# Kernel tuning notes

Measured on AMD Instinct MI355X. Metric: run time of the kernel, lower is better.

## Reference

```python
import jax, jax.numpy as jnp
import numpy as np

B, L, D = 4, 4096, 1024
H = 16
HD = D // H                      # 64
WIN = 256
MLP_RATIO = 4.0
FFN = int(2 * int(D * MLP_RATIO) / 3)   # 2730
EPS = 1e-6


def setup_inputs() -> dict:
    key = jax.random.key(0)
    ks = jax.random.split(key, 16)
    s = 0.02
    return {
        "x": jax.random.normal(ks[0], (B, L, D), jnp.float32),
        "c": jax.random.normal(ks[1], (B, D), jnp.float32),
        "norm1_scale": jnp.ones((D,), jnp.float32),
        "norm2_scale": jnp.ones((D,), jnp.float32),
        "adaLN_w": jax.random.normal(ks[2], (D, 6 * D), jnp.float32) * s,
        "adaLN_b": jnp.zeros((6 * D,), jnp.float32),
        "qkv_w": jax.random.normal(ks[3], (D, 3 * D), jnp.float32) * s,
        "qkv_b": jnp.zeros((3 * D,), jnp.float32),
        "out_proj_w": jax.random.normal(ks[4], (D, D), jnp.float32) * s,
        "out_proj_b": jnp.zeros((D,), jnp.float32),
        "w12_w": jax.random.normal(ks[5], (D, 2 * FFN), jnp.float32) * s,
        "w12_b": jnp.zeros((2 * FFN,), jnp.float32),
        "w3_w": jax.random.normal(ks[6], (FFN, D), jnp.float32) * s,
        "w3_b": jnp.zeros((D,), jnp.float32),
    }


def _rmsnorm(x, scale):
    xf = x.astype(jnp.float32)
    var = jnp.mean(jnp.square(xf), axis=-1, keepdims=True)
    xn = (xf * jax.lax.rsqrt(var + EPS)).astype(x.dtype)
    return xn * scale


def _modulation(x, shift, scale):
    return x * (1.0 + scale[:, None, :]) + shift[:, None, :]


def _rope(x):
    # Faithful to original: seq axis is x.shape[-2], which here is the HEAD axis.
    seq_len, hd = x.shape[-2], x.shape[-1]
    theta = 10000.0
    freqs = 1.0 / theta ** (jnp.arange(0, hd, 2, dtype=jnp.float32) / hd)
    t = jnp.arange(seq_len, dtype=jnp.float32)
    freqs_cis = jnp.einsum("i,j->ij", t, freqs)        # (seq, hd/2)
    sin = jnp.repeat(jnp.sin(freqs_cis), 2, axis=-1)   # (seq, hd)
    cos = jnp.repeat(jnp.cos(freqs_cis), 2, axis=-1)
    x1, x2 = jnp.split(x, 2, axis=-1)
    rot = jnp.concatenate([-x2, x1], axis=-1)
    return x * cos + rot * sin


def reference(x, c, norm1_scale, norm2_scale, adaLN_w, adaLN_b,
              qkv_w, qkv_b, out_proj_w, out_proj_b,
              w12_w, w12_b, w3_w, w3_b):
    # adaLN modulation params from conditioning
    ada = jax.nn.silu(c) @ adaLN_w + adaLN_b                      # (B, 6D)
    sh_msa, sc_msa, g_msa, sh_mlp, sc_mlp, g_mlp = jnp.split(ada, 6, axis=-1)

    # --- attention branch ---
    res = x
    xm = _modulation(_rmsnorm(x, norm1_scale), sh_msa, sc_msa)    # (B,L,D)
    nw = L // WIN
    xw = xm.reshape(B * nw, WIN, D)
    qkv = xw @ qkv_w + qkv_b
    q, k, v = jnp.split(qkv, 3, axis=-1)
    q = q.reshape(B * nw, WIN, H, HD)
    k = k.reshape(B * nw, WIN, H, HD)
    v = v.reshape(B * nw, WIN, H, HD)
    q, k = _rope(q), _rope(k)
    scores = jnp.einsum("bqhd,bkhd->bhqk", q, k) / jnp.sqrt(jnp.float32(HD))
    attn = jax.nn.softmax(scores, axis=-1)
    out = jnp.einsum("bhqk,bkhd->bqhd", attn, v).reshape(B, L, D)
    out = out @ out_proj_w + out_proj_b
    x = res + g_msa[:, None, :] * out

    # --- MLP branch ---
    res = x
    xm = _modulation(_rmsnorm(x, norm2_scale), sh_mlp, sc_mlp)
    w12 = xm @ w12_w + w12_b                                      # (B,L,2*FFN)
    w1, w2 = jnp.split(w12, 2, axis=-1)
    mlp = (jax.nn.silu(w1) * w2) @ w3_w + w3_b
    return res + g_mlp[:, None, :] * mlp
```

## Files before the change

kernel.cpp:

```cpp
#include <hip/hip_runtime.h>
#include <hip/hip_bf16.h>
#include <cstdint>
#include <cstddef>

#define DEV __device__ __forceinline__

typedef float f32x4 __attribute__((ext_vector_type(4)));
typedef short s16x8 __attribute__((ext_vector_type(8)));
typedef short s16x4 __attribute__((ext_vector_type(4)));
typedef __bf16 bf16x8 __attribute__((ext_vector_type(8)));

DEV unsigned short f2bf(float f) {
  union { float f; unsigned u; } v; v.f = f;
  return (unsigned short)((v.u + 0x7FFFu + ((v.u >> 16) & 1u)) >> 16);
}
DEV float bf2f(unsigned short s) {
  union { unsigned u; float f; } v; v.u = ((unsigned)s) << 16;
  return v.f;
}

DEV void mfma16(f32x4& d, const s16x8& a, const s16x8& b) {
  d = __builtin_amdgcn_mfma_f32_16x16x32_bf16(
      __builtin_bit_cast(bf16x8, a), __builtin_bit_cast(bf16x8, b), d, 0, 0, 0);
}

typedef const unsigned int gu32 __attribute__((address_space(1)));
typedef unsigned int lu32 __attribute__((address_space(3)));
DEV void gl_lds16(const void* g, void* l) {
  __builtin_amdgcn_global_load_lds((gu32*)g, (lu32*)l, 16, 0, 0);
}

__global__ void transpose_w(const float* __restrict__ src, int srcLd, int K,
                            int colOff, int nCols,
                            unsigned short* __restrict__ dst, int dstLd, int rowOff,
                            int ilv)
{
  __shared__ float tile[32][33];
  int tx = threadIdx.x & 31, ty = threadIdx.x >> 5;
  int k0 = blockIdx.y * 32, n0 = blockIdx.x * 32;
#pragma unroll
  for (int r = 0; r < 4; ++r) {
    int kk = k0 + ty + r * 8;
    int nn = n0 + tx;
    if (kk < K && nn < nCols) tile[ty + r * 8][tx] = src[(size_t)kk * srcLd + colOff + nn];
  }
  __syncthreads();
#pragma unroll
  for (int r = 0; r < 4; ++r) {
    int nn = n0 + ty + r * 8;
    int kk = k0 + tx;
    if (nn < nCols && kk < K) {
      int row = ilv ? (((nn >> 4) << 5) + (nn & 15) + rowOff) : (rowOff + nn);
      dst[(size_t)row * dstLd + kk] = f2bf(tile[tx][ty + r * 8]);
    }
  }
}

__global__ void biaspad_kernel(const float* __restrict__ b, float* __restrict__ out)
{
  int n = blockIdx.x * 256 + threadIdx.x;
  if (n >= 5632) return;
  int bb = n >> 4, i = n & 15;
  int src = ((bb >> 1) << 4) + i;
  float v = 0.f;
  if (src < 2730) v = (bb & 1) ? b[2730 + src] : b[src];
  out[n] = v;
}

__global__ void ada_kernel(const float* __restrict__ c, const float* __restrict__ w,
                           const float* __restrict__ b, float* __restrict__ ada)
{
  __shared__ float cs[1024];
  int bb = blockIdx.y;
  int j = blockIdx.x * 256 + threadIdx.x;
  for (int i = threadIdx.x; i < 1024; i += 256) {
    float v = c[bb * 1024 + i];
    cs[i] = v / (1.f + __expf(-v));
  }
  __syncthreads();
  float acc = b[j];
  for (int k = 0; k < 1024; ++k) acc = fmaf(cs[k], w[(size_t)k * 6144 + j], acc);
  ada[bb * 6144 + j] = acc;
}

__global__ void rmsmod_kernel(const float* __restrict__ x, const float* __restrict__ nsc,
                              const float* __restrict__ ada, int shOff, int scOff,
                              unsigned short* __restrict__ out)
{
  int row = blockIdx.x;
  int t = threadIdx.x;
  const f32x4* xr = (const f32x4*)(x + (size_t)row * 1024);
  f32x4 v = xr[t];
  float ss = v[0]*v[0] + v[1]*v[1] + v[2]*v[2] + v[3]*v[3];
#pragma unroll
  for (int off = 32; off >= 1; off >>= 1) ss += __shfl_xor(ss, off, 64);
  __shared__ float red[4];
  int lane = t & 63, wv = t >> 6;
  if (lane == 0) red[wv] = ss;
  __syncthreads();
  float tot = red[0] + red[1] + red[2] + red[3];
  float rms = rsqrtf(tot * (1.f / 1024.f) + 1e-6f);
  int bb = row >> 12;
  const float* ab = ada + bb * 6144;
  s16x4 o;
#pragma unroll
  for (int i = 0; i < 4; ++i) {
    int col = t * 4 + i;
    float xn = v[i] * rms * nsc[col];
    float val = xn * (1.f + ab[scOff + col]) + ab[shOff + col];
    o[i] = (short)f2bf(val);
  }
  *(s16x4*)(out + (size_t)row * 1024 + t * 4) = o;
}

template<int EPI>
__global__ __launch_bounds__(512, 2) void gemm256(
    const unsigned short* __restrict__ A, int lda,
    const unsigned short* __restrict__ BT, int ldb,
    int N, int K,
    const float* __restrict__ bias,
    void* __restrict__ Cout, int Nout,
    const float* __restrict__ res,
    const float* __restrict__ ada, int gateOff)
{
  __shared__ __align__(16) char lds[131072];

  const int tid = threadIdx.x;
  const int lane = tid & 63;
  const int wv = tid >> 6;
  const int wr = wv >> 2;
  const int wn = wv & 3;
  const int g = lane >> 4, r16 = lane & 15;

  const int nwg = gridDim.x * gridDim.y;
  const int bid = blockIdx.x + gridDim.x * blockIdx.y;
  const int qq = nwg >> 3;
  const int swz = (bid & 7) * qq + (bid >> 3);
  const int m0 = (swz / gridDim.x) * 256;
  const int n0 = (swz % gridDim.x) * 256;

  const int nkt = K >> 6;

  auto stageB = [&](int t) {
    if (t >= nkt) return;
    const int bs = t & 1;
#pragma unroll
    for (int it = 0; it < 4; ++it) {
      const int cidx = it * 512 + tid;
      const int rl = cidx >> 3, cc = cidx & 7;
      const unsigned short* src =
          BT + (size_t)(n0 + rl) * ldb + t * 64 + ((cc ^ (rl & 7)) << 3);
      gl_lds16(src, lds + 65536 + bs * 32768 + cidx * 16);
    }
  };
  auto stageA = [&](int t) {
    if (t >= nkt) return;
    const int bs = t & 1;
#pragma unroll
    for (int it = 0; it < 4; ++it) {
      const int cidx = it * 512 + tid;
      const int rl = cidx >> 3, cc = cidx & 7;
      const unsigned short* src =
          A + (size_t)(m0 + rl) * lda + t * 64 + ((cc ^ (rl & 7)) << 3);
      gl_lds16(src, lds + bs * 32768 + cidx * 16);
    }
  };

  f32x4 acc[8][4];
#pragma unroll
  for (int m = 0; m < 8; ++m)
#pragma unroll
    for (int n = 0; n < 4; ++n) { acc[m][n][0]=0.f; acc[m][n][1]=0.f; acc[m][n][2]=0.f; acc[m][n][3]=0.f; }

  int swzk[2];
#pragma unroll
  for (int ks = 0; ks < 2; ++ks) swzk[ks] = (((ks << 2) + g) ^ (r16 & 7)) << 4;
  int arow0[4], arow1[4], brow0[2], brow1[2];
#pragma unroll
  for (int m = 0; m < 4; ++m) {
    arow0[m] = (wr * 128 + m * 16 + r16) * 128;
    arow1[m] = (wr * 128 + 64 + m * 16 + r16) * 128;
  }
#pragma unroll
  for (int n = 0; n < 2; ++n) {
    brow0[n] = 65536 + (wn * 64 + n * 16 + r16) * 128;
    brow1[n] = 65536 + (wn * 64 + 32 + n * 16 + r16) * 128;
  }

  stageB(0); stageA(0); stageB(1); stageA(1);
  asm volatile("s_waitcnt vmcnt(8)" ::: "memory");
  __builtin_amdgcn_s_barrier();

  for (int kt = 0; kt < nkt; ++kt) {
    const int boff = (kt & 1) * 32768;
    s16x8 a0[4][2], a1[4][2], b0[2][2], b1[2][2];
#pragma unroll
    for (int m = 0; m < 4; ++m)
#pragma unroll
      for (int ks = 0; ks < 2; ++ks)
        a0[m][ks] = *(const s16x8*)(lds + boff + arow0[m] + swzk[ks]);
#pragma unroll
    for (int n = 0; n < 2; ++n)
#pragma unroll
      for (int ks = 0; ks < 2; ++ks)
        b0[n][ks] = *(const s16x8*)(lds + boff + brow0[n] + swzk[ks]);
#pragma unroll
    for (int n = 0; n < 2; ++n)
#pragma unroll
      for (int ks = 0; ks < 2; ++ks)
        b1[n][ks] = *(const s16x8*)(lds + boff + brow1[n] + swzk[ks]);
#pragma unroll
    for (int m = 0; m < 4; ++m)
#pragma unroll
      for (int ks = 0; ks < 2; ++ks)
        a1[m][ks] = *(const s16x8*)(lds + boff + arow1[m] + swzk[ks]);
    __builtin_amdgcn_s_setprio(1);
#pragma unroll
    for (int m = 0; m < 4; ++m)
#pragma unroll
      for (int n = 0; n < 2; ++n)
#pragma unroll
        for (int ks = 0; ks < 2; ++ks)
          mfma16(acc[m][n], a0[m][ks], b0[n][ks]);
    __builtin_amdgcn_s_setprio(0);
    __builtin_amdgcn_s_setprio(1);
#pragma unroll
    for (int m = 0; m < 4; ++m)
#pragma unroll
      for (int n = 0; n < 2; ++n)
#pragma unroll
        for (int ks = 0; ks < 2; ++ks)
          mfma16(acc[m][2 + n], a0[m][ks], b1[n][ks]);
    __builtin_amdgcn_s_setprio(0);
    __builtin_amdgcn_s_barrier();
    stageB(kt + 2);
    __builtin_amdgcn_s_setprio(1);
#pragma unroll
    for (int m = 0; m < 4; ++m)
#pragma unroll
      for (int n = 0; n < 2; ++n)
#pragma unroll
        for (int ks = 0; ks < 2; ++ks)
          mfma16(acc[4 + m][2 + n], a1[m][ks], b1[n][ks]);
    __builtin_amdgcn_s_setprio(0);
    if (kt + 2 < nkt) asm volatile("s_waitcnt vmcnt(4)" ::: "memory");
    else              asm volatile("s_waitcnt vmcnt(0)" ::: "memory");
    __builtin_amdgcn_s_barrier();
    stageA(kt + 2);
    __builtin_amdgcn_s_setprio(1);
#pragma unroll
    for (int m = 0; m < 4; ++m)
#pragma unroll
      for (int n = 0; n < 2; ++n)
#pragma unroll
        for (int ks = 0; ks < 2; ++ks)
          mfma16(acc[4 + m][n], a1[m][ks], b0[n][ks]);
    __builtin_amdgcn_s_setprio(0);
  }

  if (EPI == 0) {
    unsigned short* Co = (unsigned short*)Cout;
#pragma unroll
    for (int fm = 0; fm < 8; ++fm)
#pragma unroll
      for (int fn = 0; fn < 4; ++fn)
#pragma unroll
        for (int r = 0; r < 4; ++r) {
          int rg = m0 + wr * 128 + fm * 16 + g * 4 + r;
          int cg = n0 + wn * 64 + fn * 16 + r16;
          Co[(size_t)rg * Nout + cg] = f2bf(acc[fm][fn][r] + bias[cg]);
        }
  } else if (EPI == 1) {
    unsigned short* Co = (unsigned short*)Cout;
#pragma unroll
    for (int fm = 0; fm < 8; ++fm)
#pragma unroll
      for (int p = 0; p < 2; ++p)
#pragma unroll
        for (int r = 0; r < 4; ++r) {
          int rg = m0 + wr * 128 + fm * 16 + g * 4 + r;
          int cg = n0 + wn * 64 + (2 * p) * 16 + r16;
          float v1 = acc[fm][2 * p][r] + bias[cg];
          float v2 = acc[fm][2 * p + 1][r] + bias[cg + 16];
          float h = v1 / (1.f + __expf(-v1)) * v2;
          int hcol = (n0 >> 1) + wn * 32 + p * 16 + r16;
          Co[(size_t)rg * Nout + hcol] = f2bf(h);
        }
  } else {
    float* Co = (float*)Cout;
#pragma unroll
    for (int fm = 0; fm < 8; ++fm)
#pragma unroll
      for (int fn = 0; fn < 4; ++fn)
#pragma unroll
        for (int r = 0; r < 4; ++r) {
          int rg = m0 + wr * 128 + fm * 16 + g * 4 + r;
          int cg = n0 + wn * 64 + fn * 16 + r16;
          float v = acc[fm][fn][r] + bias[cg];
          int bb = rg >> 12;
          float gate = ada[bb * 6144 + gateOff + cg];
          size_t idx = (size_t)rg * Nout + cg;
          Co[idx] = res[idx] + gate * v;
        }
  }
}

template<int MODE>
__global__ void gemm128(const unsigned short* __restrict__ A, int lda,
                        const unsigned short* __restrict__ BT,
                        int N, int K,
                        const float* __restrict__ bias,
                        void* __restrict__ Cout,
                        const float* __restrict__ res,
                        const float* __restrict__ ada, int gateOff, int mOff)
{
  __shared__ __align__(16) unsigned short As[128 * 32];
  __shared__ __align__(16) unsigned short Bs[128 * 32];

  const int tid = threadIdx.x;
  const int lane = tid & 63;
  const int wv = tid >> 6;
  const int wr = wv >> 1, wc = wv & 1;
  const int g = lane >> 4, r16 = lane & 15;
  const int m0 = blockIdx.y * 128, n0 = blockIdx.x * 128;

  const int c0 = tid, c1 = 256 + tid;
  const int ra0 = c0 >> 2, ra1 = c1 >> 2;
  const int k0 = ((c0 & 3) ^ ((ra0 >> 1) & 3)) * 8;
  const int k1 = ((c1 & 3) ^ ((ra1 >> 1) & 3)) * 8;
  const unsigned short* ga0 = A + (size_t)(m0 + ra0) * lda + k0;
  const unsigned short* ga1 = A + (size_t)(m0 + ra1) * lda + k1;
  const unsigned short* gb0 = BT + (size_t)(n0 + ra0) * K + k0;
  const unsigned short* gb1 = BT + (size_t)(n0 + ra1) * K + k1;
  unsigned short* la0 = As + c0 * 8;
  unsigned short* la1 = As + c1 * 8;
  unsigned short* lb0 = Bs + c0 * 8;
  unsigned short* lb1 = Bs + c1 * 8;

  f32x4 acc[4][4];
#pragma unroll
  for (int m = 0; m < 4; ++m)
#pragma unroll
    for (int n = 0; n < 4; ++n) { acc[m][n][0]=0.f; acc[m][n][1]=0.f; acc[m][n][2]=0.f; acc[m][n][3]=0.f; }

  int aoff[4], boff[4];
#pragma unroll
  for (int m = 0; m < 4; ++m) {
    int rl = wr * 64 + m * 16 + r16;
    aoff[m] = rl * 32 + (g ^ ((rl >> 1) & 3)) * 8;
    int rb = wc * 64 + m * 16 + r16;
    boff[m] = rb * 32 + (g ^ ((rb >> 1) & 3)) * 8;
  }

  const int nk = K >> 5;
  for (int kt = 0; kt < nk; ++kt) {
    __syncthreads();
    const int ko = kt * 32;
    gl_lds16(ga0 + ko, la0);
    gl_lds16(ga1 + ko, la1);
    gl_lds16(gb0 + ko, lb0);
    gl_lds16(gb1 + ko, lb1);
    __syncthreads();
    s16x8 af[4], bf[4];
#pragma unroll
    for (int m = 0; m < 4; ++m) af[m] = *(const s16x8*)(As + aoff[m]);
#pragma unroll
    for (int n = 0; n < 4; ++n) bf[n] = *(const s16x8*)(Bs + boff[n]);
#pragma unroll
    for (int m = 0; m < 4; ++m)
#pragma unroll
      for (int n = 0; n < 4; ++n) mfma16(acc[m][n], af[m], bf[n]);
  }

#pragma unroll
  for (int m = 0; m < 4; ++m) {
#pragma unroll
    for (int n = 0; n < 4; ++n) {
#pragma unroll
      for (int r = 0; r < 4; ++r) {
        int rg = m0 + wr * 64 + m * 16 + g * 4 + r;
        int cg = n0 + wc * 64 + n * 16 + r16;
        float v = acc[m][n][r] + bias[cg];
        size_t idx = (size_t)rg * N + cg;
        if (MODE == 0 || MODE == 2) {
          ((unsigned short*)Cout)[idx] = f2bf(v);
        } else {
          int bb = (mOff + rg) >> 12;
          float gate = ada[bb * 6144 + gateOff + cg];
          ((float*)Cout)[idx] = res[idx] + gate * v;
        }
      }
    }
  }
}

__global__ void vtrans_kernel(const unsigned short* __restrict__ qkv,
                              unsigned short* __restrict__ vT)
{
  __shared__ unsigned short tl[64][72];
  int pidx = blockIdx.x;
  int w = pidx >> 4, h = pidx & 15;
  int t = threadIdx.x;
  for (int jb = 0; jb < 4; ++jb) {
    int jl = t >> 2, dc = t & 3;
    const unsigned short* srcp =
        qkv + (size_t)(w * 256 + jb * 64 + jl) * 3072 + 2048 + h * 64 + dc * 16;
    s16x8 v0 = *(const s16x8*)(srcp);
    s16x8 v1 = *(const s16x8*)(srcp + 8);
    if (jb) __syncthreads();
    *(s16x8*)(&tl[jl][dc * 16]) = v0;
    *(s16x8*)(&tl[jl][dc * 16 + 8]) = v1;
    __syncthreads();
    int dl = t >> 2, jc = t & 3;
    s16x8 o0, o1;
#pragma unroll
    for (int i = 0; i < 8; ++i) {
      o0[i] = (short)tl[jc * 16 + i][dl];
      o1[i] = (short)tl[jc * 16 + 8 + i][dl];
    }
    unsigned short* dstp = vT + (size_t)pidx * (64 * 256) + (size_t)dl * 256 + jb * 64 + jc * 16;
    *(s16x8*)(dstp) = o0;
    *(s16x8*)(dstp + 8) = o1;
  }
}

__global__ __launch_bounds__(256, 1) void attn_kernel(
    const unsigned short* __restrict__ qkv,
    const unsigned short* __restrict__ vT,
    unsigned short* __restrict__ attnout)
{
  __shared__ __align__(16) unsigned short Kl[256 * 64];
  __shared__ __align__(16) unsigned short Vl[64 * 256];
  __shared__ __align__(16) unsigned short Pl[4][64 * 88];

  const int tid = threadIdx.x;
  const int lane = tid & 63;
  const int wv = tid >> 6;
  const int g = lane >> 4, r16 = lane & 15;
  const int p = blockIdx.x;
  const int w = p >> 4, h = p & 15;
  const float hh = (float)h;
  const float F = 0.4152410118609203f;

#pragma unroll
  for (int it = 0; it < 4; ++it) {
    int idx = it * 256 + tid;
    int j = idx >> 2;
    int c = idx & 3;
    const unsigned short* kg = qkv + (size_t)(w * 256 + j) * 3072 + 1024 + h * 64;
    s16x8 lo = *(const s16x8*)(kg + c * 8);
    s16x8 hi = *(const s16x8*)(kg + 32 + c * 8);
    s16x8 plo, phi;
#pragma unroll
    for (int i2 = 0; i2 < 4; ++i2) {
      float f1 = exp2f(-(float)(c * 4 + i2) * F);
      float f2 = exp2f(-(float)(16 + c * 4 + i2) * F);
      float s1, c1s, s2, c2s;
      sincosf(hh * f1, &s1, &c1s);
      sincosf(hh * f2, &s2, &c2s);
#pragma unroll
      for (int u = 0; u < 2; ++u) {
        int i = i2 * 2 + u;
        float a = bf2f((unsigned short)lo[i]);
        float b = bf2f((unsigned short)hi[i]);
        plo[i] = (short)f2bf(a * c1s - b * s1);
        phi[i] = (short)f2bf(b * c2s + a * s2);
      }
    }
    int swzL = c ^ (j & 7);
    int swzH = (c + 4) ^ (j & 7);
    *(s16x8*)(Kl + j * 64 + swzL * 8) = plo;
    *(s16x8*)(Kl + j * 64 + swzH * 8) = phi;
  }
  {
    const unsigned short* vg = vT + (size_t)p * (64 * 256);
#pragma unroll
    for (int it = 0; it < 8; ++it) {
      int idx = it * 256 + tid;
      int d = idx >> 5;
      int c = idx & 31;
      s16x8 val = *(const s16x8*)(vg + d * 256 + c * 8);
      int cs = (c & ~7) | ((c ^ d) & 7);
      *(s16x8*)(Vl + d * 256 + cs * 8) = val;
    }
  }

  s16x8 qa[4][2];
  {
    float cs0[4], sn0[4], cs1[4], sn1[4];
#pragma unroll
    for (int i2 = 0; i2 < 4; ++i2) {
      float f1 = exp2f(-(float)(g * 4 + i2) * F);
      float f2 = exp2f(-(float)(16 + g * 4 + i2) * F);
      sincosf(hh * f1, &sn0[i2], &cs0[i2]);
      sincosf(hh * f2, &sn1[i2], &cs1[i2]);
    }
#pragma unroll
    for (int m = 0; m < 4; ++m) {
      const unsigned short* qg =
          qkv + (size_t)(w * 256 + wv * 64 + m * 16 + r16) * 3072 + h * 64;
      s16x8 lo = *(const s16x8*)(qg + g * 8);
      s16x8 hi = *(const s16x8*)(qg + 32 + g * 8);
      s16x8 plo, phi;
#pragma unroll
      for (int i = 0; i < 8; ++i) {
        int i2 = i >> 1;
        float a = bf2f((unsigned short)lo[i]);
        float b = bf2f((unsigned short)hi[i]);
        plo[i] = (short)f2bf(a * cs0[i2] - b * sn0[i2]);
        phi[i] = (short)f2bf(b * cs1[i2] + a * sn1[i2]);
      }
      qa[m][0] = plo;
      qa[m][1] = phi;
    }
  }

  __syncthreads();

  f32x4 accO[4][4];
  float Mx[4][4], Ls[4][4];
#pragma unroll
  for (int m = 0; m < 4; ++m)
#pragma unroll
    for (int r = 0; r < 4; ++r) {
      Mx[m][r] = -3.0e38f;
      Ls[m][r] = 0.f;
      accO[m][r][0]=0.f; accO[m][r][1]=0.f; accO[m][r][2]=0.f; accO[m][r][3]=0.f;
    }
  unsigned short* Pw = &Pl[wv][0];
  const float zs = 0.125f * 1.44269504f;

  for (int kb = 0; kb < 4; ++kb) {
    f32x4 s[4][4];
#pragma unroll
    for (int m = 0; m < 4; ++m)
#pragma unroll
      for (int jt = 0; jt < 4; ++jt) { s[m][jt][0]=0.f; s[m][jt][1]=0.f; s[m][jt][2]=0.f; s[m][jt][3]=0.f; }

#pragma unroll
    for (int jt = 0; jt < 4; ++jt) {
      int j = kb * 64 + jt * 16 + r16;
      s16x8 bk0 = *(const s16x8*)(Kl + j * 64 + ((g ^ (j & 7)) * 8));
      s16x8 bk1 = *(const s16x8*)(Kl + j * 64 + (((4 + g) ^ (j & 7)) * 8));
#pragma unroll
      for (int m = 0; m < 4; ++m) {
        mfma16(s[m][jt], qa[m][0], bk0);
        mfma16(s[m][jt], qa[m][1], bk1);
      }
    }

#pragma unroll
    for (int m = 0; m < 4; ++m) {
#pragma unroll
      for (int r = 0; r < 4; ++r) {
        float mx = fmaxf(fmaxf(s[m][0][r], s[m][1][r]), fmaxf(s[m][2][r], s[m][3][r]));
        mx = fmaxf(mx, __shfl_xor(mx, 1, 16));
        mx = fmaxf(mx, __shfl_xor(mx, 2, 16));
        mx = fmaxf(mx, __shfl_xor(mx, 4, 16));
        mx = fmaxf(mx, __shfl_xor(mx, 8, 16));
        float Mn = fmaxf(Mx[m][r], mx * zs);
        float fsc = exp2f(Mx[m][r] - Mn);
        Mx[m][r] = Mn;
        float ps = 0.f;
#pragma unroll
        for (int jt = 0; jt < 4; ++jt) {
          float pv = exp2f(s[m][jt][r] * zs - Mn);
          s[m][jt][r] = pv;
          ps += pv;
        }
        ps += __shfl_xor(ps, 1, 16);
        ps += __shfl_xor(ps, 2, 16);
        ps += __shfl_xor(ps, 4, 16);
        ps += __shfl_xor(ps, 8, 16);
        Ls[m][r] = Ls[m][r] * fsc + ps;
#pragma unroll
        for (int dt = 0; dt < 4; ++dt) accO[m][dt][r] *= fsc;
      }
    }

#pragma unroll
    for (int m = 0; m < 4; ++m)
#pragma unroll
      for (int jt = 0; jt < 4; ++jt)
#pragma unroll
        for (int r = 0; r < 4; ++r) {
          int q = m * 16 + g * 4 + r;
          int jj = jt * 16 + r16;
          Pw[q * 88 + jj] = f2bf(s[m][jt][r]);
        }
    asm volatile("s_waitcnt lgkmcnt(0)" ::: "memory");
    __builtin_amdgcn_sched_barrier(0);

#pragma unroll
    for (int c = 0; c < 2; ++c) {
      s16x8 pa[4];
#pragma unroll
      for (int m = 0; m < 4; ++m)
        pa[m] = *(const s16x8*)(Pw + (m * 16 + r16) * 88 + c * 32 + g * 8);
#pragma unroll
      for (int dt = 0; dt < 4; ++dt) {
        int d = dt * 16 + r16;
        int cch = kb * 8 + c * 4 + g;
        int csz = (cch & ~7) | ((cch ^ d) & 7);
        s16x8 vb = *(const s16x8*)(Vl + d * 256 + csz * 8);
#pragma unroll
        for (int m = 0; m < 4; ++m) mfma16(accO[m][dt], pa[m], vb);
      }
    }
    asm volatile("s_waitcnt lgkmcnt(0)" ::: "memory");
    __builtin_amdgcn_sched_barrier(0);
  }

#pragma unroll
  for (int m = 0; m < 4; ++m)
#pragma unroll
    for (int dt = 0; dt < 4; ++dt)
#pragma unroll
      for (int r = 0; r < 4; ++r) {
        int rg = w * 256 + wv * 64 + m * 16 + g * 4 + r;
        int cg = h * 64 + dt * 16 + r16;
        float val = accO[m][dt][r] / Ls[m][r];
        attnout[(size_t)rg * 1024 + cg] = f2bf(val);
      }
}

extern "C" void kernel_launch(void* const* d_in, const int* in_sizes, int n_in,
                              void* d_out, int out_size, void* d_ws, size_t ws_size,
                              hipStream_t stream)
{
  const float* x    = (const float*)d_in[0];
  const float* c    = (const float*)d_in[1];
  const float* n1s  = (const float*)d_in[2];
  const float* n2s  = (const float*)d_in[3];
  const float* adaW = (const float*)d_in[4];
  const float* adaB = (const float*)d_in[5];
  const float* qkvW = (const float*)d_in[6];
  const float* qkvB = (const float*)d_in[7];
  const float* outW = (const float*)d_in[8];
  const float* outB = (const float*)d_in[9];
  const float* w12W = (const float*)d_in[10];
  const float* w12B = (const float*)d_in[11];
  const float* w3W  = (const float*)d_in[12];
  const float* w3B  = (const float*)d_in[13];

  char* ws = (char*)d_ws;
  constexpr size_t OFF_ADA  = 0;
  constexpr size_t OFF_QKVT = 98304;
  constexpr size_t OFF_OUTT = OFF_QKVT + 6291456;
  constexpr size_t OFF_W12T = OFF_OUTT + 2097152;
  constexpr size_t OFF_W3T  = OFF_W12T + 11534336;
  constexpr size_t OFF_BPAD = OFF_W3T + 5767168;
  constexpr size_t OFF_XM   = OFF_BPAD + 22528;
  constexpr size_t OFF_BIG  = OFF_XM + 33554432;
  constexpr size_t OFF_QKVC = OFF_BIG;
  constexpr size_t OFF_VTC  = OFF_BIG + 50331648;
  constexpr size_t OFF_ATTC = OFF_BIG + 67108864;
  constexpr size_t OFF_HBUF = OFF_BIG;

  float* ada            = (float*)(ws + OFF_ADA);
  unsigned short* qkvT  = (unsigned short*)(ws + OFF_QKVT);
  unsigned short* outT  = (unsigned short*)(ws + OFF_OUTT);
  unsigned short* w12T  = (unsigned short*)(ws + OFF_W12T);
  unsigned short* w3T   = (unsigned short*)(ws + OFF_W3T);
  float* biasPad        = (float*)(ws + OFF_BPAD);
  unsigned short* xm    = (unsigned short*)(ws + OFF_XM);
  unsigned short* qkvbC = (unsigned short*)(ws + OFF_QKVC);
  unsigned short* vTbC  = (unsigned short*)(ws + OFF_VTC);
  unsigned short* attnC = (unsigned short*)(ws + OFF_ATTC);
  unsigned short* hbuf  = (unsigned short*)(ws + OFF_HBUF);
  float* x2             = (float*)d_out;

  hipMemsetAsync(w12T, 0, 11534336, stream);
  hipMemsetAsync(w3T, 0, 5767168, stream);
  transpose_w<<<dim3(96, 32), 256, 0, stream>>>(qkvW, 3072, 1024, 0, 3072, qkvT, 1024, 0, 0);
  transpose_w<<<dim3(32, 32), 256, 0, stream>>>(outW, 1024, 1024, 0, 1024, outT, 1024, 0, 0);
  transpose_w<<<dim3(86, 32), 256, 0, stream>>>(w12W, 5460, 1024, 0, 2730, w12T, 1024, 0, 1);
  transpose_w<<<dim3(86, 32), 256, 0, stream>>>(w12W, 5460, 1024, 2730, 2730, w12T, 1024, 16, 1);
  transpose_w<<<dim3(32, 86), 256, 0, stream>>>(w3W, 1024, 2730, 0, 1024, w3T, 2816, 0, 0);
  biaspad_kernel<<<22, 256, 0, stream>>>(w12B, biasPad);
  ada_kernel<<<dim3(24, 4), 256, 0, stream>>>(c, adaW, adaB, ada);

  rmsmod_kernel<<<16384, 256, 0, stream>>>(x, n1s, ada, 0, 1024, xm);
  for (int ch = 0; ch < 2; ++ch) {
    const size_t ro = (size_t)ch * 8192;
    gemm256<0><<<dim3(12, 32), 512, 0, stream>>>(
        xm + ro * 1024, 1024, qkvT, 1024, 3072, 1024, qkvB, qkvbC, 3072,
        nullptr, nullptr, 0);
    vtrans_kernel<<<512, 256, 0, stream>>>(qkvbC, vTbC);
    attn_kernel<<<512, 256, 0, stream>>>(qkvbC, vTbC, attnC);
    gemm128<1><<<dim3(8, 64), 256, 0, stream>>>(
        attnC, 1024, outT, 1024, 1024, outB, x2 + ro * 1024, x + ro * 1024,
        ada, 2048, (int)ro);
  }

  rmsmod_kernel<<<16384, 256, 0, stream>>>(x2, n2s, ada, 3072, 4096, xm);
  gemm256<1><<<dim3(22, 64), 512, 0, stream>>>(
      xm, 1024, w12T, 1024, 5632, 1024, biasPad, hbuf, 2816,
      nullptr, nullptr, 0);
  gemm256<2><<<dim3(4, 64), 512, 0, stream>>>(
      hbuf, 2816, w3T, 2816, 1024, 2816, w3B, x2, 1024,
      x2, ada, 5120);
}
```

Measured before the change: 763.8 us.

## Switch gemm256 to 32x32x16 MFMA and fuse V transpose into QKV epilogue

Rewrites the 256x256 GEMM inner loop to use 32x32x16 bf16 MFMA tiles instead of 16x16x32, which changes the fragment layout, LDS read offsets, and the w12 interleave and bias padding (now 32-column groups). The QKV GEMM epilogue now writes the V part directly in transposed per-window, per-head layout, so the separate vtrans kernel and its extra pass over V are removed. The larger MFMA shape should reduce LDS fragment reads per flop. In exchange the transposed V stores are scattered 2-byte writes, and the wait count and accumulator register pressure change.

```diff
diff --git a/kernel.cpp b/kernel.cpp
--- a/kernel.cpp
+++ b/kernel.cpp
@@ -6,6 +6,7 @@
 #define DEV __device__ __forceinline__
 
 typedef float f32x4 __attribute__((ext_vector_type(4)));
+typedef float f32x16 __attribute__((ext_vector_type(16)));
 typedef short s16x8 __attribute__((ext_vector_type(8)));
 typedef short s16x4 __attribute__((ext_vector_type(4)));
 typedef __bf16 bf16x8 __attribute__((ext_vector_type(8)));
@@ -21,6 +22,10 @@
 
 DEV void mfma16(f32x4& d, const s16x8& a, const s16x8& b) {
   d = __builtin_amdgcn_mfma_f32_16x16x32_bf16(
+      __builtin_bit_cast(bf16x8, a), __builtin_bit_cast(bf16x8, b), d, 0, 0, 0);
+}
+DEV void mfma32(f32x16& d, const s16x8& a, const s16x8& b) {
+  d = __builtin_amdgcn_mfma_f32_32x32x16_bf16(
       __builtin_bit_cast(bf16x8, a), __builtin_bit_cast(bf16x8, b), d, 0, 0, 0);
 }
 
@@ -50,7 +55,7 @@
     int nn = n0 + ty + r * 8;
     int kk = k0 + tx;
     if (nn < nCols && kk < K) {
-      int row = ilv ? (((nn >> 4) << 5) + (nn & 15) + rowOff) : (rowOff + nn);
+      int row = ilv ? (((nn >> 5) << 6) + (nn & 31) + rowOff) : (rowOff + nn);
       dst[(size_t)row * dstLd + kk] = f2bf(tile[tx][ty + r * 8]);
     }
   }
@@ -60,10 +65,10 @@
 {
   int n = blockIdx.x * 256 + threadIdx.x;
   if (n >= 5632) return;
-  int bb = n >> 4, i = n & 15;
-  int src = ((bb >> 1) << 4) + i;
+  int bb = n >> 6, w = n & 63;
+  int src = bb * 32 + (w & 31);
   float v = 0.f;
-  if (src < 2730) v = (bb & 1) ? b[2730 + src] : b[src];
+  if (src < 2730) v = (w < 32) ? b[src] : b[2730 + src];
   out[n] = v;
 }
 
@@ -121,7 +126,8 @@
     const float* __restrict__ bias,
     void* __restrict__ Cout, int Nout,
     const float* __restrict__ res,
-    const float* __restrict__ ada, int gateOff)
+    const float* __restrict__ ada, int gateOff,
+    unsigned short* __restrict__ vTout)
 {
   __shared__ __align__(16) char lds[131072];
 
@@ -130,7 +136,7 @@
   const int wv = tid >> 6;
   const int wr = wv >> 2;
   const int wn = wv & 3;
-  const int g = lane >> 4, r16 = lane & 15;
+  const int l31 = lane & 31, hi = lane >> 5;
 
   const int nwg = gridDim.x * gridDim.y;
   const int bid = blockIdx.x + gridDim.x * blockIdx.y;
@@ -166,26 +172,22 @@
     }
   };
 
-  f32x4 acc[8][4];
-#pragma unroll
-  for (int m = 0; m < 8; ++m)
-#pragma unroll
-    for (int n = 0; n < 4; ++n) { acc[m][n][0]=0.f; acc[m][n][1]=0.f; acc[m][n][2]=0.f; acc[m][n][3]=0.f; }
-
-  int swzk[2];
-#pragma unroll
-  for (int ks = 0; ks < 2; ++ks) swzk[ks] = (((ks << 2) + g) ^ (r16 & 7)) << 4;
-  int arow0[4], arow1[4], brow0[2], brow1[2];
-#pragma unroll
-  for (int m = 0; m < 4; ++m) {
-    arow0[m] = (wr * 128 + m * 16 + r16) * 128;
-    arow1[m] = (wr * 128 + 64 + m * 16 + r16) * 128;
-  }
-#pragma unroll
-  for (int n = 0; n < 2; ++n) {
-    brow0[n] = 65536 + (wn * 64 + n * 16 + r16) * 128;
-    brow1[n] = 65536 + (wn * 64 + 32 + n * 16 + r16) * 128;
-  }
+  f32x16 acc[4][2];
+#pragma unroll
+  for (int m = 0; m < 4; ++m)
+#pragma unroll
+    for (int n = 0; n < 2; ++n)
+#pragma unroll
+      for (int i = 0; i < 16; ++i) acc[m][n][i] = 0.f;
+
+  int koffs[4];
+#pragma unroll
+  for (int ks = 0; ks < 4; ++ks) koffs[ks] = (((ks * 2 + hi) ^ (lane & 7)) << 4);
+  int abase[4], bbase[2];
+#pragma unroll
+  for (int fm = 0; fm < 4; ++fm) abase[fm] = (wr * 128 + fm * 32 + l31) * 128;
+#pragma unroll
+  for (int fn = 0; fn < 2; ++fn) bbase[fn] = 65536 + (wn * 64 + fn * 32 + l31) * 128;
 
   stageB(0); stageA(0); stageB(1); stageA(1);
   asm volatile("s_waitcnt vmcnt(8)" ::: "memory");
@@ -193,115 +195,116 @@
 
   for (int kt = 0; kt < nkt; ++kt) {
     const int boff = (kt & 1) * 32768;
-    s16x8 a0[4][2], a1[4][2], b0[2][2], b1[2][2];
-#pragma unroll
-    for (int m = 0; m < 4; ++m)
-#pragma unroll
-      for (int ks = 0; ks < 2; ++ks)
-        a0[m][ks] = *(const s16x8*)(lds + boff + arow0[m] + swzk[ks]);
-#pragma unroll
-    for (int n = 0; n < 2; ++n)
-#pragma unroll
-      for (int ks = 0; ks < 2; ++ks)
-        b0[n][ks] = *(const s16x8*)(lds + boff + brow0[n] + swzk[ks]);
-#pragma unroll
-    for (int n = 0; n < 2; ++n)
-#pragma unroll
-      for (int ks = 0; ks < 2; ++ks)
-        b1[n][ks] = *(const s16x8*)(lds + boff + brow1[n] + swzk[ks]);
-#pragma unroll
-    for (int m = 0; m < 4; ++m)
-#pragma unroll
-      for (int ks = 0; ks < 2; ++ks)
-        a1[m][ks] = *(const s16x8*)(lds + boff + arow1[m] + swzk[ks]);
+    s16x8 a0[2][4], a1[2][4], b0[4], b1[4];
+#pragma unroll
+    for (int fm = 0; fm < 2; ++fm)
+#pragma unroll
+      for (int ks = 0; ks < 4; ++ks)
+        a0[fm][ks] = *(const s16x8*)(lds + boff + abase[fm] + koffs[ks]);
+#pragma unroll
+    for (int ks = 0; ks < 4; ++ks)
+      b0[ks] = *(const s16x8*)(lds + boff + bbase[0] + koffs[ks]);
     __builtin_amdgcn_s_setprio(1);
 #pragma unroll
-    for (int m = 0; m < 4; ++m)
-#pragma unroll
-      for (int n = 0; n < 2; ++n)
-#pragma unroll
-        for (int ks = 0; ks < 2; ++ks)
-          mfma16(acc[m][n], a0[m][ks], b0[n][ks]);
+    for (int fm = 0; fm < 2; ++fm)
+#pragma unroll
+      for (int ks = 0; ks < 4; ++ks)
+        mfma32(acc[fm][0], a0[fm][ks], b0[ks]);
     __builtin_amdgcn_s_setprio(0);
+#pragma unroll
+    for (int ks = 0; ks < 4; ++ks)
+      b1[ks] = *(const s16x8*)(lds + boff + bbase[1] + koffs[ks]);
     __builtin_amdgcn_s_setprio(1);
 #pragma unroll
-    for (int m = 0; m < 4; ++m)
-#pragma unroll
-      for (int n = 0; n < 2; ++n)
-#pragma unroll
-        for (int ks = 0; ks < 2; ++ks)
-          mfma16(acc[m][2 + n], a0[m][ks], b1[n][ks]);
+    for (int fm = 0; fm < 2; ++fm)
+#pragma unroll
+      for (int ks = 0; ks < 4; ++ks)
+        mfma32(acc[fm][1], a0[fm][ks], b1[ks]);
     __builtin_amdgcn_s_setprio(0);
     __builtin_amdgcn_s_barrier();
     stageB(kt + 2);
+#pragma unroll
+    for (int fm = 0; fm < 2; ++fm)
+#pragma unroll
+      for (int ks = 0; ks < 4; ++ks)
+        a1[fm][ks] = *(const s16x8*)(lds + boff + abase[2 + fm] + koffs[ks]);
     __builtin_amdgcn_s_setprio(1);
 #pragma unroll
-    for (int m = 0; m < 4; ++m)
-#pragma unroll
-      for (int n = 0; n < 2; ++n)
-#pragma unroll
-        for (int ks = 0; ks < 2; ++ks)
-          mfma16(acc[4 + m][2 + n], a1[m][ks], b1[n][ks]);
+    for (int fm = 0; fm < 2; ++fm)
+#pragma unroll
+      for (int ks = 0; ks < 4; ++ks)
+        mfma32(acc[2 + fm][1], a1[fm][ks], b1[ks]);
     __builtin_amdgcn_s_setprio(0);
-    if (kt + 2 < nkt) asm volatile("s_waitcnt vmcnt(4)" ::: "memory");
+    if (kt + 2 < nkt) asm volatile("s_waitcnt vmcnt(8)" ::: "memory");
     else              asm volatile("s_waitcnt vmcnt(0)" ::: "memory");
     __builtin_amdgcn_s_barrier();
     stageA(kt + 2);
     __builtin_amdgcn_s_setprio(1);
 #pragma unroll
-    for (int m = 0; m < 4; ++m)
-#pragma unroll
-      for (int n = 0; n < 2; ++n)
-#pragma unroll
-        for (int ks = 0; ks < 2; ++ks)
-          mfma16(acc[4 + m][n], a1[m][ks], b0[n][ks]);
+    for (int fm = 0; fm < 2; ++fm)
+#pragma unroll
+      for (int ks = 0; ks < 4; ++ks)
+        mfma32(acc[2 + fm][0], a1[fm][ks], b0[ks]);
     __builtin_amdgcn_s_setprio(0);
   }
 
-  if (EPI == 0) {
+  if (EPI == 1) {
     unsigned short* Co = (unsigned short*)Cout;
-#pragma unroll
-    for (int fm = 0; fm < 8; ++fm)
-#pragma unroll
-      for (int fn = 0; fn < 4; ++fn)
-#pragma unroll
-        for (int r = 0; r < 4; ++r) {
-          int rg = m0 + wr * 128 + fm * 16 + g * 4 + r;
-          int cg = n0 + wn * 64 + fn * 16 + r16;
-          Co[(size_t)rg * Nout + cg] = f2bf(acc[fm][fn][r] + bias[cg]);
-        }
-  } else if (EPI == 1) {
-    unsigned short* Co = (unsigned short*)Cout;
-#pragma unroll
-    for (int fm = 0; fm < 8; ++fm)
-#pragma unroll
-      for (int p = 0; p < 2; ++p)
-#pragma unroll
-        for (int r = 0; r < 4; ++r) {
-          int rg = m0 + wr * 128 + fm * 16 + g * 4 + r;
-          int cg = n0 + wn * 64 + (2 * p) * 16 + r16;
-          float v1 = acc[fm][2 * p][r] + bias[cg];
-          float v2 = acc[fm][2 * p + 1][r] + bias[cg + 16];
-          float h = v1 / (1.f + __expf(-v1)) * v2;
-          int hcol = (n0 >> 1) + wn * 32 + p * 16 + r16;
-          Co[(size_t)rg * Nout + hcol] = f2bf(h);
-        }
-  } else {
+    const int cgl = n0 + wn * 64 + l31;
+    const int hcol = (n0 >> 1) + wn * 32 + l31;
+    const float bs1 = bias[cgl], bs2 = bias[cgl + 32];
+#pragma unroll
+    for (int fm = 0; fm < 4; ++fm)
+#pragma unroll
+      for (int reg = 0; reg < 16; ++reg) {
+        int rg = m0 + wr * 128 + fm * 32 + (reg & 3) + 8 * (reg >> 2) + 4 * hi;
+        float v1 = acc[fm][0][reg] + bs1;
+        float v2 = acc[fm][1][reg] + bs2;
+        float h = v1 / (1.f + __expf(-v1)) * v2;
+        Co[(size_t)rg * Nout + hcol] = f2bf(h);
+      }
+  } else if (EPI == 2) {
     float* Co = (float*)Cout;
 #pragma unroll
-    for (int fm = 0; fm < 8; ++fm)
-#pragma unroll
-      for (int fn = 0; fn < 4; ++fn)
-#pragma unroll
-        for (int r = 0; r < 4; ++r) {
-          int rg = m0 + wr * 128 + fm * 16 + g * 4 + r;
-          int cg = n0 + wn * 64 + fn * 16 + r16;
-          float v = acc[fm][fn][r] + bias[cg];
+    for (int fm = 0; fm < 4; ++fm)
+#pragma unroll
+      for (int fn = 0; fn < 2; ++fn) {
+        int cg = n0 + wn * 64 + fn * 32 + l31;
+        float bs = bias[cg];
+#pragma unroll
+        for (int reg = 0; reg < 16; ++reg) {
+          int rg = m0 + wr * 128 + fm * 32 + (reg & 3) + 8 * (reg >> 2) + 4 * hi;
+          float v = acc[fm][fn][reg] + bs;
           int bb = rg >> 12;
           float gate = ada[bb * 6144 + gateOff + cg];
           size_t idx = (size_t)rg * Nout + cg;
           Co[idx] = res[idx] + gate * v;
         }
+      }
+  } else {
+    unsigned short* Co = (unsigned short*)Cout;
+#pragma unroll
+    for (int fm = 0; fm < 4; ++fm)
+#pragma unroll
+      for (int fn = 0; fn < 2; ++fn) {
+        int cg = n0 + wn * 64 + fn * 32 + l31;
+        float bs = bias[cg];
+        if (cg < 2048) {
+#pragma unroll
+          for (int reg = 0; reg < 16; ++reg) {
+            int rg = m0 + wr * 128 + fm * 32 + (reg & 3) + 8 * (reg >> 2) + 4 * hi;
+            Co[(size_t)rg * Nout + cg] = f2bf(acc[fm][fn][reg] + bs);
+          }
+        } else {
+          int h = (cg - 2048) >> 6, d = (cg - 2048) & 63;
+          unsigned short* vbase = vTout + ((size_t)((m0 >> 8) * 16 + h)) * 16384 + d * 256;
+#pragma unroll
+          for (int reg = 0; reg < 16; ++reg) {
+            int rg = m0 + wr * 128 + fm * 32 + (reg & 3) + 8 * (reg >> 2) + 4 * hi;
+            vbase[rg & 255] = f2bf(acc[fm][fn][reg] + bs);
+          }
+        }
+      }
   }
 }
 
@@ -391,36 +394,6 @@
         }
       }
     }
-  }
-}
-
-__global__ void vtrans_kernel(const unsigned short* __restrict__ qkv,
-                              unsigned short* __restrict__ vT)
-{
-  __shared__ unsigned short tl[64][72];
-  int pidx = blockIdx.x;
-  int w = pidx >> 4, h = pidx & 15;
-  int t = threadIdx.x;
-  for (int jb = 0; jb < 4; ++jb) {
-    int jl = t >> 2, dc = t & 3;
-    const unsigned short* srcp =
-        qkv + (size_t)(w * 256 + jb * 64 + jl) * 3072 + 2048 + h * 64 + dc * 16;
-    s16x8 v0 = *(const s16x8*)(srcp);
-    s16x8 v1 = *(const s16x8*)(srcp + 8);
-    if (jb) __syncthreads();
-    *(s16x8*)(&tl[jl][dc * 16]) = v0;
-    *(s16x8*)(&tl[jl][dc * 16 + 8]) = v1;
-    __syncthreads();
-    int dl = t >> 2, jc = t & 3;
-    s16x8 o0, o1;
-#pragma unroll
-    for (int i = 0; i < 8; ++i) {
-      o0[i] = (short)tl[jc * 16 + i][dl];
-      o1[i] = (short)tl[jc * 16 + 8 + i][dl];
-    }
-    unsigned short* dstp = vT + (size_t)pidx * (64 * 256) + (size_t)dl * 256 + jb * 64 + jc * 16;
-    *(s16x8*)(dstp) = o0;
-    *(s16x8*)(dstp + 8) = o1;
   }
 }
 
@@ -675,7 +648,7 @@
   transpose_w<<<dim3(96, 32), 256, 0, stream>>>(qkvW, 3072, 1024, 0, 3072, qkvT, 1024, 0, 0);
   transpose_w<<<dim3(32, 32), 256, 0, stream>>>(outW, 1024, 1024, 0, 1024, outT, 1024, 0, 0);
   transpose_w<<<dim3(86, 32), 256, 0, stream>>>(w12W, 5460, 1024, 0, 2730, w12T, 1024, 0, 1);
-  transpose_w<<<dim3(86, 32), 256, 0, stream>>>(w12W, 5460, 1024, 2730, 2730, w12T, 1024, 16, 1);
+  transpose_w<<<dim3(86, 32), 256, 0, stream>>>(w12W, 5460, 1024, 2730, 2730, w12T, 1024, 32, 1);
   transpose_w<<<dim3(32, 86), 256, 0, stream>>>(w3W, 1024, 2730, 0, 1024, w3T, 2816, 0, 0);
   biaspad_kernel<<<22, 256, 0, stream>>>(w12B, biasPad);
   ada_kernel<<<dim3(24, 4), 256, 0, stream>>>(c, adaW, adaB, ada);
@@ -683,10 +656,9 @@
   rmsmod_kernel<<<16384, 256, 0, stream>>>(x, n1s, ada, 0, 1024, xm);
   for (int ch = 0; ch < 2; ++ch) {
     const size_t ro = (size_t)ch * 8192;
-    gemm256<0><<<dim3(12, 32), 512, 0, stream>>>(
+    gemm256<3><<<dim3(12, 32), 512, 0, stream>>>(
         xm + ro * 1024, 1024, qkvT, 1024, 3072, 1024, qkvB, qkvbC, 3072,
-        nullptr, nullptr, 0);
-    vtrans_kernel<<<512, 256, 0, stream>>>(qkvbC, vTbC);
+        nullptr, nullptr, 0, vTbC);
     attn_kernel<<<512, 256, 0, stream>>>(qkvbC, vTbC, attnC);
     gemm128<1><<<dim3(8, 64), 256, 0, stream>>>(
         attnC, 1024, outT, 1024, 1024, outB, x2 + ro * 1024, x + ro * 1024,
@@ -696,8 +668,8 @@
   rmsmod_kernel<<<16384, 256, 0, stream>>>(x2, n2s, ada, 3072, 4096, xm);
   gemm256<1><<<dim3(22, 64), 512, 0, stream>>>(
       xm, 1024, w12T, 1024, 5632, 1024, biasPad, hbuf, 2816,
-      nullptr, nullptr, 0);
+      nullptr, nullptr, 0, nullptr);
   gemm256<2><<<dim3(4, 64), 512, 0, stream>>>(
       hbuf, 2816, w3T, 2816, 1024, 2816, w3B, x2, 1024,
-      x2, ada, 5120);
-}
+      x2, ada, 5120, nullptr);
+}
```

Result: slower. 803.6 us (+5.2%).
